# Kernel optimization log

Hardware: AMD Instinct MI355X
Metric: run time of the kernel (lower is better)

Reference implementation:

```python
import jax, jax.numpy as jnp
import numpy as np

HIDDEN = 1024
N_HEADS = 16
HEAD_DIM = HIDDEN // N_HEADS
B, S = 4, 4096


def setup_inputs() -> dict:
    key = jax.random.key(0)
    k1, k2, k3, k4, k5 = jax.random.split(key, 5)
    hidden_states = jax.random.normal(k1, (B, S, HIDDEN), dtype=jnp.float32)
    attention_mask = jnp.zeros((B, 1, 1, S), dtype=jnp.float32)
    scale = 1.0 / np.sqrt(HIDDEN)
    Wq = jax.random.normal(k2, (HIDDEN, HIDDEN), dtype=jnp.float32) * scale
    bq = jax.random.normal(k3, (HIDDEN,), dtype=jnp.float32) * 0.01
    Wkv = jax.random.normal(k4, (HIDDEN, HIDDEN), dtype=jnp.float32) * scale
    bkv = jax.random.normal(k5, (HIDDEN,), dtype=jnp.float32) * 0.01
    return {"hidden_states": hidden_states, "attention_mask": attention_mask,
            "Wq": Wq, "bq": bq, "Wkv": Wkv, "bkv": bkv}


def _split_heads(x, b, s):
    # [B, S, HIDDEN] -> [B, H, S, D]
    return x.reshape(b, s, N_HEADS, HEAD_DIM).transpose(0, 2, 1, 3)


def reference(hidden_states, attention_mask, Wq, bq, Wkv, bkv):
    b, s, _ = hidden_states.shape
    inv_sqrt_d = 1.0 / np.sqrt(HEAD_DIM)

    q = _split_heads(hidden_states @ Wq + bq, b, s)     # [B,H,S,D]
    k = _split_heads(hidden_states @ Wkv + bkv, b, s)   # [B,H,S,D]; value == key

    # ---- global token (index 0) attends to everything ----
    gq = q[:, :, 0:1, :]                                              # [B,H,1,D]
    g_scores = jnp.einsum('bhqd,bhkd->bhqk', gq, k) * inv_sqrt_d + attention_mask
    g_attn = jax.nn.softmax(g_scores, axis=-1)                        # [B,H,1,S]
    g_vec = jnp.einsum('bhqk,bhkd->bhqd', g_attn, k)                  # [B,H,1,D]

    # ---- local tokens 1..S-1: keys = [self, global_vec, prev, next(wrap to 0)] ----
    k_self = k[:, :, 1:, :]                                           # [B,H,S-1,D]
    k_glob = jnp.broadcast_to(g_vec, k_self.shape)                    # [B,H,S-1,D]
    k_prev = k[:, :, :-1, :]                                          # [B,H,S-1,D]
    k_next = jnp.concatenate([k[:, :, 2:, :], k[:, :, 0:1, :]], axis=2)
    keys4 = jnp.stack([k_self, k_glob, k_prev, k_next], axis=-1)      # [B,H,S-1,D,4]

    l_scores = jnp.einsum('bhsd,bhsdk->bhsk', q[:, :, 1:, :], keys4) * inv_sqrt_d
    l_attn = jax.nn.softmax(l_scores, axis=-1)                        # [B,H,S-1,4]
    l_vec = jnp.einsum('bhsk,bhsdk->bhsd', l_attn, keys4)             # [B,H,S-1,D]

    context = jnp.concatenate([g_vec, l_vec], axis=2)                 # [B,H,S,D]
    context = context.transpose(0, 2, 1, 3).reshape(b, s, N_HEADS * HEAD_DIM)
    return context, l_attn[:, :, :, None, :]                          # [B,H,S-1,1,4]
```

## Files before the change

### kernel.cpp

```cpp
#include <hip/hip_runtime.h>
#include <hip/hip_bf16.h>

#define NHEADS 16
#define HDIM   64
#define HID    1024
#define BB     4
#define SS     4096
#define MM     (BB*SS)
#define KK     HID
#define NN     (2*HID)

using short8 = __attribute__((ext_vector_type(8))) short;
using f32x4  = __attribute__((ext_vector_type(4))) float;

__device__ __forceinline__ float bf2f(ushort u) {
  return __uint_as_float(((unsigned)u) << 16);
}
__device__ __forceinline__ ushort f2bf(float f) {
  unsigned u = __float_as_uint(f);
  unsigned r = (u + 0x7fffu + ((u >> 16) & 1u)) >> 16;
  return (ushort)r;
}

__device__ __forceinline__ void gload16(const void* g, void* l) {
  __builtin_amdgcn_global_load_lds(
      (const __attribute__((address_space(1))) void*)g,
      (__attribute__((address_space(3))) void*)l, 16, 0, 0);
}

__global__ __launch_bounds__(256) void cast_hs_k(const float* __restrict__ in,
                                                 ushort* __restrict__ out) {
  size_t i = ((size_t)blockIdx.x * 256 + threadIdx.x) * 8;
  float4 a = *(const float4*)(in + i);
  float4 b = *(const float4*)(in + i + 4);
  ushort r[8];
  r[0]=f2bf(a.x); r[1]=f2bf(a.y); r[2]=f2bf(a.z); r[3]=f2bf(a.w);
  r[4]=f2bf(b.x); r[5]=f2bf(b.y); r[6]=f2bf(b.z); r[7]=f2bf(b.w);
  *(uint4*)(out + i) = *(const uint4*)r;
}

__global__ __launch_bounds__(256) void wcast_k(const float* __restrict__ Wq,
                                               const float* __restrict__ Wkv,
                                               ushort* __restrict__ Bt) {
  __shared__ float tile[32][33];
  int k0 = blockIdx.x * 32, n0 = blockIdx.y * 32;
  int tx = threadIdx.x, ty = threadIdx.y;
  const float* src = (n0 < HID) ? Wq : Wkv;
  int nc = (n0 < HID) ? n0 : n0 - HID;
#pragma unroll
  for (int j = 0; j < 4; ++j)
    tile[ty + 8*j][tx] = src[(size_t)(k0 + ty + 8*j) * HID + nc + tx];
  __syncthreads();
#pragma unroll
  for (int j = 0; j < 4; ++j)
    Bt[(size_t)(n0 + ty + 8*j) * KK + k0 + tx] = f2bf(tile[tx][ty + 8*j]);
}

__global__ __launch_bounds__(512, 2) void gemm_k(const ushort* __restrict__ A,
                                                 const ushort* __restrict__ Bt,
                                                 const float* __restrict__ bq,
                                                 const float* __restrict__ bkv,
                                                 ushort* __restrict__ C) {
  extern __shared__ char lds_c[];
  const int tid = threadIdx.x;
  const int bid = blockIdx.x;
  const int wg = (bid & 7) * 64 + (bid >> 3);
  const int tm = wg >> 3, tn = wg & 7;
  const int w = tid >> 6, lane = tid & 63;
  const int wr = w >> 2, wc = w & 3;
  const int lr = lane & 15, hi = lane >> 4;

  const ushort* Ab = A  + (size_t)tm * 256 * KK;
  const ushort* Bb = Bt + (size_t)tn * 256 * KK;

  const int d0 = tid * 16;
  const int gch = (tid & 3) ^ ((tid >> 3) & 3);
  const size_t soff0 = (size_t)(tid >> 2) * KK + gch * 8;
  const size_t soff1 = soff0 + (size_t)128 * KK;

  const int swz = (hi ^ ((lr >> 1) & 3)) << 4;
  const int arow = (wr * 128 + lr) * 64 + swz;
  const int brow = (wc * 64 + lr) * 64 + swz;

  f32x4 acc[8][4];
#pragma unroll
  for (int M = 0; M < 8; ++M)
#pragma unroll
    for (int n = 0; n < 4; ++n) acc[M][n] = (f32x4){0.f, 0.f, 0.f, 0.f};
  short8 bfrag[4];

#define STG(PANEL, KOFF, DSTB)                                                  \
  {                                                                             \
    const ushort* g_ = (PANEL) + (KOFF);                                        \
    gload16(g_ + soff0, lds_c + (DSTB) + d0);                                   \
    gload16(g_ + soff1, lds_c + (DSTB) + 8192 + d0);                            \
  }

#define LOADB(BBASE)                                                            \
  _Pragma("unroll") for (int n = 0; n < 4; ++n)                                 \
    bfrag[n] = *(const short8*)(lds_c + (BBASE) + n * 1024 + brow);

#define WAITV(N)                                                                \
  { asm volatile("s_waitcnt vmcnt(" #N ")" ::: "memory");                       \
    __builtin_amdgcn_sched_barrier(0); }

#define PH(ABASE, MH, STAGE_CODE, TAIL_CODE)                                    \
  {                                                                             \
    short8 afrag[4];                                                            \
    _Pragma("unroll") for (int m = 0; m < 4; ++m)                               \
      afrag[m] = *(const short8*)(lds_c + (ABASE) + (MH) * 4096 +               \
                                  m * 1024 + arow);                             \
    STAGE_CODE;                                                                 \
    __builtin_amdgcn_s_barrier();                                               \
    __builtin_amdgcn_sched_barrier(0);     \
    __builtin_amdgcn_s_setprio(1);                                              \
    _Pragma("unroll") for (int m = 0; m < 4; ++m)                               \
      _Pragma("unroll") for (int n = 0; n < 4; ++n)                             \
        acc[(MH) * 4 + m][n] = __builtin_amdgcn_mfma_f32_16x16x32_bf16(         \
            bfrag[n], afrag[m], acc[(MH) * 4 + m][n], 0, 0, 0);                 \
    __builtin_amdgcn_s_setprio(0);                                              \
    TAIL_CODE;                                                                  \
    __builtin_amdgcn_s_barrier();                                               \
    asm volatile("" ::: "memory");                                              \
  }

  STG(Bb, 0,   32768);
  STG(Ab, 0,   0);
  STG(Bb, 32,  49152);
  STG(Ab, 32,  16384);
  STG(Bb, 64,  98304);
  STG(Ab, 64,  65536);
  WAITV(8)
  __builtin_amdgcn_s_barrier();
  asm volatile("" ::: "memory");

#pragma unroll 1
  for (int it = 0; it < 7; ++it) {
    LOADB(32768)
    PH(0, 0, STG(Bb, (2 * it + 1) * 64 + 32, 114688), {})
    PH(0, 1, STG(Ab, (2 * it + 1) * 64 + 32, 81920), WAITV(8))
    LOADB(49152)
    PH(16384, 0, STG(Bb, (2 * it + 2) * 64, 32768), {})
    PH(16384, 1, STG(Ab, (2 * it + 2) * 64, 0), WAITV(8))
    LOADB(98304)
    PH(65536, 0, STG(Bb, (2 * it + 2) * 64 + 32, 49152), {})
    PH(65536, 1, STG(Ab, (2 * it + 2) * 64 + 32, 16384), WAITV(8))
    LOADB(114688)
    PH(81920, 0, STG(Bb, (2 * it + 3) * 64, 98304), {})
    PH(81920, 1, STG(Ab, (2 * it + 3) * 64, 65536), WAITV(8))
  }
  LOADB(32768)
  PH(0, 0, STG(Bb, 15 * 64 + 32, 114688), {})
  PH(0, 1, STG(Ab, 15 * 64 + 32, 81920), WAITV(8))
  LOADB(49152)
  PH(16384, 0, {}, {})
  PH(16384, 1, {}, WAITV(4))
  LOADB(98304)
  PH(65536, 0, {}, {})
  PH(65536, 1, {}, WAITV(0))
  LOADB(114688)
  PH(81920, 0, {}, {})
  PH(81920, 1, {}, {})

#undef PH
#undef WAITV
#undef LOADB
#undef STG

  const float* bias = (tn < 4) ? (bq + tn * 256) : (bkv + (tn - 4) * 256);
  float4 bv[4];
#pragma unroll
  for (int n = 0; n < 4; ++n)
    bv[n] = *(const float4*)(bias + wc * 64 + n * 16 + hi * 4);

#pragma unroll
  for (int M = 0; M < 8; ++M) {
    size_t row = (size_t)tm * 256 + wr * 128 + M * 16 + lr;
    ushort* cp = C + row * NN + tn * 256 + wc * 64 + hi * 4;
#pragma unroll
    for (int n = 0; n < 4; ++n) {
      unsigned p0 = (unsigned)f2bf(acc[M][n][0] + bv[n].x) |
                    ((unsigned)f2bf(acc[M][n][1] + bv[n].y) << 16);
      unsigned p1 = (unsigned)f2bf(acc[M][n][2] + bv[n].z) |
                    ((unsigned)f2bf(acc[M][n][3] + bv[n].w) << 16);
      uint2 st; st.x = p0; st.y = p1;
      *(uint2*)(cp + n * 16) = st;
    }
  }
}

#define GCH 8
#define GCS (SS / GCH)

__global__ __launch_bounds__(512) void gattn_part_k(const ushort* __restrict__ QK,
                                                    const float* __restrict__ mask,
                                                    float* __restrict__ P) {
  const int bh = blockIdx.x >> 3, c = blockIdx.x & 7;
  const int b = bh >> 4, h = bh & 15;
  const int tid = threadIdx.x, w = tid >> 6, lane = tid & 63;
  __shared__ float sc[GCS];
  __shared__ float red[8];
  __shared__ float vacc[8][64];

  const float gq = bf2f(QK[(size_t)b * SS * NN + h * HDIM + lane]);
  const int s0 = c * GCS;
  float mx = -1e30f;
  for (int s = w; s < GCS; s += 8) {
    float kv = bf2f(QK[((size_t)b * SS + s0 + s) * NN + HID + h * HDIM + lane]);
    float p = gq * kv;
#pragma unroll
    for (int o = 32; o; o >>= 1) p += __shfl_xor(p, o, 64);
    p = p * 0.125f + mask[b * SS + s0 + s];
    if (lane == 0) sc[s] = p;
    mx = fmaxf(mx, p);
  }
  if (lane == 0) red[w] = mx;
  __syncthreads();
  float bm = -1e30f;
#pragma unroll
  for (int i = 0; i < 8; ++i) bm = fmaxf(bm, red[i]);
  __syncthreads();
  float ls = 0.f;
  for (int s = tid; s < GCS; s += 512) {
    float e = __expf(sc[s] - bm);
    sc[s] = e;
    ls += e;
  }
#pragma unroll
  for (int o = 32; o; o >>= 1) ls += __shfl_xor(ls, o, 64);
  if (lane == 0) red[w] = ls;
  __syncthreads();
  float tot = 0.f;
#pragma unroll
  for (int i = 0; i < 8; ++i) tot += red[i];

  float a = 0.f;
  for (int s = w; s < GCS; s += 8)
    a += sc[s] * bf2f(QK[((size_t)b * SS + s0 + s) * NN + HID + h * HDIM + lane]);
  vacc[w][lane] = a;
  __syncthreads();
  if (w == 0) {
    float v = 0.f;
#pragma unroll
    for (int i = 0; i < 8; ++i) v += vacc[i][lane];
    P[1024 + (bh * 8 + c) * 64 + lane] = v;
    if (lane == 0) {
      P[bh * 8 + c] = bm;
      P[512 + bh * 8 + c] = tot;
    }
  }
}

__global__ __launch_bounds__(64) void gattn_comb_k(const float* __restrict__ P,
                                                   float* __restrict__ ctx,
                                                   float* __restrict__ gvec) {
  const int bh = blockIdx.x, b = bh >> 4, h = bh & 15;
  const int lane = threadIdx.x;
  float pm[8];
  float m = -1e30f;
#pragma unroll
  for (int c = 0; c < 8; ++c) { pm[c] = P[bh * 8 + c]; m = fmaxf(m, pm[c]); }
  float tot = 0.f, g = 0.f;
#pragma unroll
  for (int c = 0; c < 8; ++c) {
    float e = __expf(pm[c] - m);
    tot += P[512 + bh * 8 + c] * e;
    g += P[1024 + (bh * 8 + c) * 64 + lane] * e;
  }
  g /= tot;
  gvec[b * HID + h * HDIM + lane] = g;
  ctx[(size_t)b * SS * HID + h * HDIM + lane] = g;
}

__device__ __forceinline__ void unpack16(const ushort* __restrict__ p, float* f) {
  uint4 v0 = *(const uint4*)p;
  uint4 v1 = *(const uint4*)(p + 8);
  unsigned u[8] = {v0.x, v0.y, v0.z, v0.w, v1.x, v1.y, v1.z, v1.w};
#pragma unroll
  for (int i = 0; i < 8; ++i) {
    f[2*i]   = __uint_as_float(u[i] << 16);
    f[2*i+1] = __uint_as_float(u[i] & 0xffff0000u);
  }
}

__global__ __launch_bounds__(256) void local_attn_k(const ushort* __restrict__ QK,
                                                    const float* __restrict__ gvec,
                                                    float* __restrict__ out) {
  const int blk = blockIdx.x;
  const int b = blk >> 10;
  const int s = 1 + ((blk & 1023) << 2) + (int)(threadIdx.x >> 6);
  if (s >= SS) return;
  const int lane = threadIdx.x & 63;
  const int g = lane >> 2, j = lane & 3;
  const int db = g*HDIM + j*16;

  const size_t base = ((size_t)b*SS + s) * NN;
  const ushort* qp  = QK + base + db;
  const ushort* ksp = QK + base + HID + db;
  const ushort* kpp = QK + base - NN + HID + db;
  const int sn = (s == SS-1) ? 0 : s + 1;
  const ushort* knp = QK + ((size_t)b*SS + sn)*NN + HID + db;
  const float*  gvp = gvec + b*HID + db;

  float q[16], ks[16], kp[16], kn[16], gv[16];
  unpack16(qp, q); unpack16(ksp, ks); unpack16(kpp, kp); unpack16(knp, kn);
#pragma unroll
  for (int t = 0; t < 16; t += 4) *(float4*)(gv + t) = *(const float4*)(gvp + t);

  float d0=0.f, d1=0.f, d2=0.f, d3=0.f;
#pragma unroll
  for (int t = 0; t < 16; ++t) {
    d0 += q[t]*ks[t]; d1 += q[t]*gv[t]; d2 += q[t]*kp[t]; d3 += q[t]*kn[t];
  }
  d0 += __shfl_xor(d0, 1, 64); d0 += __shfl_xor(d0, 2, 64);
  d1 += __shfl_xor(d1, 1, 64); d1 += __shfl_xor(d1, 2, 64);
  d2 += __shfl_xor(d2, 1, 64); d2 += __shfl_xor(d2, 2, 64);
  d3 += __shfl_xor(d3, 1, 64); d3 += __shfl_xor(d3, 2, 64);

  float s0 = d0*0.125f, s1 = d1*0.125f, s2 = d2*0.125f, s3 = d3*0.125f;
  float m = fmaxf(fmaxf(s0, s1), fmaxf(s2, s3));
  float e0 = __expf(s0 - m), e1 = __expf(s1 - m), e2 = __expf(s2 - m), e3 = __expf(s3 - m);
  float inv = 1.f / (e0 + e1 + e2 + e3);
  float a0 = e0*inv, a1 = e1*inv, a2 = e2*inv, a3 = e3*inv;

  float o[16];
#pragma unroll
  for (int t = 0; t < 16; ++t) o[t] = a0*ks[t] + a1*gv[t] + a2*kp[t] + a3*kn[t];
  float* cp = out + ((size_t)b*SS + s)*HID + db;
#pragma unroll
  for (int t = 0; t < 16; t += 4) *(float4*)(cp + t) = *(const float4*)(o + t);

  if (j == 0) {
    float4 av; av.x = a0; av.y = a1; av.z = a2; av.w = a3;
    *(float4*)(out + (size_t)BB*SS*HID + (((size_t)b*NHEADS + g)*(SS-1) + (s-1))*4) = av;
  }
}

extern "C" void kernel_launch(void* const* d_in, const int* in_sizes, int n_in,
                              void* d_out, int out_size, void* d_ws, size_t ws_size,
                              hipStream_t stream) {
  const float* hs   = (const float*)d_in[0];
  const float* mask = (const float*)d_in[1];
  const float* Wq   = (const float*)d_in[2];
  const float* bq   = (const float*)d_in[3];
  const float* Wkv  = (const float*)d_in[4];
  const float* bkv  = (const float*)d_in[5];
  float* out = (float*)d_out;

  char* ws = (char*)d_ws;
  ushort* hsb  = (ushort*)ws;
  ushort* Bt   = (ushort*)(ws + 33554432);
  ushort* QK   = (ushort*)(ws + 33554432 + 4194304);
  float*  gvec = (float*)(ws + 33554432 + 4194304 + 67108864);
  float*  P    = (float*)(ws + 33554432 + 4194304 + 67108864 + 16384);

  cast_hs_k<<<MM*KK/(256*8), 256, 0, stream>>>(hs, hsb);
  wcast_k<<<dim3(KK/32, NN/32), dim3(32, 8), 0, stream>>>(Wq, Wkv, Bt);
  gemm_k<<<dim3((MM/256)*(NN/256)), dim3(512), 131072, stream>>>(hsb, Bt, bq, bkv, QK);
  gattn_part_k<<<BB*NHEADS*GCH, 512, 0, stream>>>(QK, mask, P);
  gattn_comb_k<<<BB*NHEADS, 64, 0, stream>>>(P, out, gvec);
  local_attn_k<<<BB*1024, 256, 0, stream>>>(QK, gvec, out);
}
```

Measured before the change: 176.1 us.

## Pre-pack operands into MFMA fragment layout and load GEMM fragments directly from global

The cast kernels now write hidden states and weights as bf16 in a fragment-major layout that matches the 16x16x32 MFMA operand order. The GEMM drops its LDS staging, barriers and hand-scheduled pipeline, and instead loads each wave's A/B fragments directly from global memory into double-buffered registers. This removes LDS traffic and synchronization. In exchange, each block gets no shared reuse across waves, so L2/global traffic is duplicated and there is less latency hiding.

```diff
diff --git a/kernel.cpp b/kernel.cpp
--- a/kernel.cpp
+++ b/kernel.cpp
@@ -22,150 +22,93 @@
   return (ushort)r;
 }
 
-__device__ __forceinline__ void gload16(const void* g, void* l) {
-  __builtin_amdgcn_global_load_lds(
-      (const __attribute__((address_space(1))) void*)g,
-      (__attribute__((address_space(3))) void*)l, 16, 0, 0);
-}
-
-__global__ __launch_bounds__(256) void cast_hs_k(const float* __restrict__ in,
-                                                 ushort* __restrict__ out) {
-  size_t i = ((size_t)blockIdx.x * 256 + threadIdx.x) * 8;
-  float4 a = *(const float4*)(in + i);
-  float4 b = *(const float4*)(in + i + 4);
+__global__ __launch_bounds__(256) void af_cast_k(const float* __restrict__ hs,
+                                                 ushort* __restrict__ Af) {
+  const int t = threadIdx.x;
+  const int U = blockIdx.x * 4 + (t >> 6);
+  const int l = t & 63, lr = l & 15, hi = l >> 4;
+  const int mt = U >> 5, g = U & 31;
+  const float* src = hs + (size_t)(mt * 16 + lr) * HID + g * 32 + hi * 8;
+  float4 x = *(const float4*)src;
+  float4 y = *(const float4*)(src + 4);
   ushort r[8];
-  r[0]=f2bf(a.x); r[1]=f2bf(a.y); r[2]=f2bf(a.z); r[3]=f2bf(a.w);
-  r[4]=f2bf(b.x); r[5]=f2bf(b.y); r[6]=f2bf(b.z); r[7]=f2bf(b.w);
-  *(uint4*)(out + i) = *(const uint4*)r;
-}
-
-__global__ __launch_bounds__(256) void wcast_k(const float* __restrict__ Wq,
-                                               const float* __restrict__ Wkv,
-                                               ushort* __restrict__ Bt) {
+  r[0]=f2bf(x.x); r[1]=f2bf(x.y); r[2]=f2bf(x.z); r[3]=f2bf(x.w);
+  r[4]=f2bf(y.x); r[5]=f2bf(y.y); r[6]=f2bf(y.z); r[7]=f2bf(y.w);
+  *(uint4*)(Af + (size_t)U * 512 + l * 8) = *(const uint4*)r;
+}
+
+__global__ __launch_bounds__(256) void wf_cast_k(const float* __restrict__ Wq,
+                                                 const float* __restrict__ Wkv,
+                                                 ushort* __restrict__ Bf) {
   __shared__ float tile[32][33];
-  int k0 = blockIdx.x * 32, n0 = blockIdx.y * 32;
-  int tx = threadIdx.x, ty = threadIdx.y;
+  const int k0 = blockIdx.x * 32, n0 = blockIdx.y * 32;
+  const int tx = threadIdx.x & 31, ty = threadIdx.x >> 5;
   const float* src = (n0 < HID) ? Wq : Wkv;
-  int nc = (n0 < HID) ? n0 : n0 - HID;
+  const int nc = (n0 < HID) ? n0 : n0 - HID;
 #pragma unroll
   for (int j = 0; j < 4; ++j)
     tile[ty + 8*j][tx] = src[(size_t)(k0 + ty + 8*j) * HID + nc + tx];
   __syncthreads();
-#pragma unroll
-  for (int j = 0; j < 4; ++j)
-    Bt[(size_t)(n0 + ty + 8*j) * KK + k0 + tx] = f2bf(tile[tx][ty + 8*j]);
-}
-
-__global__ __launch_bounds__(512, 2) void gemm_k(const ushort* __restrict__ A,
-                                                 const ushort* __restrict__ Bt,
+  const int t = threadIdx.x;
+  if (t < 128) {
+    const int l = t & 63, h = t >> 6, lr = l & 15, hi = l >> 4;
+    const int nt = (n0 >> 4) + h, g = k0 >> 5;
+    ushort r[8];
+#pragma unroll
+    for (int e = 0; e < 8; ++e) r[e] = f2bf(tile[hi*8 + e][h*16 + lr]);
+    *(uint4*)(Bf + (size_t)(nt * 32 + g) * 512 + l * 8) = *(const uint4*)r;
+  }
+}
+
+__global__ __launch_bounds__(512, 2) void gemm_k(const ushort* __restrict__ Af,
+                                                 const ushort* __restrict__ Bf,
                                                  const float* __restrict__ bq,
                                                  const float* __restrict__ bkv,
                                                  ushort* __restrict__ C) {
-  extern __shared__ char lds_c[];
-  const int tid = threadIdx.x;
-  const int bid = blockIdx.x;
+  const int tid = threadIdx.x, bid = blockIdx.x;
   const int wg = (bid & 7) * 64 + (bid >> 3);
   const int tm = wg >> 3, tn = wg & 7;
   const int w = tid >> 6, lane = tid & 63;
   const int wr = w >> 2, wc = w & 3;
   const int lr = lane & 15, hi = lane >> 4;
 
-  const ushort* Ab = A  + (size_t)tm * 256 * KK;
-  const ushort* Bb = Bt + (size_t)tn * 256 * KK;
-
-  const int d0 = tid * 16;
-  const int gch = (tid & 3) ^ ((tid >> 3) & 3);
-  const size_t soff0 = (size_t)(tid >> 2) * KK + gch * 8;
-  const size_t soff1 = soff0 + (size_t)128 * KK;
-
-  const int swz = (hi ^ ((lr >> 1) & 3)) << 4;
-  const int arow = (wr * 128 + lr) * 64 + swz;
-  const int brow = (wc * 64 + lr) * 64 + swz;
+  const ushort* aB = Af + (size_t)(tm * 16 + wr * 8) * 16384 + lane * 8;
+  const ushort* bB = Bf + (size_t)(tn * 16 + wc * 4) * 16384 + lane * 8;
 
   f32x4 acc[8][4];
 #pragma unroll
   for (int M = 0; M < 8; ++M)
 #pragma unroll
     for (int n = 0; n < 4; ++n) acc[M][n] = (f32x4){0.f, 0.f, 0.f, 0.f};
-  short8 bfrag[4];
-
-#define STG(PANEL, KOFF, DSTB)                                                  \
-  {                                                                             \
-    const ushort* g_ = (PANEL) + (KOFF);                                        \
-    gload16(g_ + soff0, lds_c + (DSTB) + d0);                                   \
-    gload16(g_ + soff1, lds_c + (DSTB) + 8192 + d0);                            \
-  }
-
-#define LOADB(BBASE)                                                            \
+
+  short8 a0[8], a1[8], b0[4], b1[4];
+
+#define LDA(SET, G)                                                             \
+  _Pragma("unroll") for (int m = 0; m < 8; ++m)                                 \
+    SET[m] = *(const short8*)(aB + m * 16384 + (G) * 512);
+#define LDB(SET, G)                                                             \
   _Pragma("unroll") for (int n = 0; n < 4; ++n)                                 \
-    bfrag[n] = *(const short8*)(lds_c + (BBASE) + n * 1024 + brow);
-
-#define WAITV(N)                                                                \
-  { asm volatile("s_waitcnt vmcnt(" #N ")" ::: "memory");                       \
-    __builtin_amdgcn_sched_barrier(0); }
-
-#define PH(ABASE, MH, STAGE_CODE, TAIL_CODE)                                    \
-  {                                                                             \
-    short8 afrag[4];                                                            \
-    _Pragma("unroll") for (int m = 0; m < 4; ++m)                               \
-      afrag[m] = *(const short8*)(lds_c + (ABASE) + (MH) * 4096 +               \
-                                  m * 1024 + arow);                             \
-    STAGE_CODE;                                                                 \
-    __builtin_amdgcn_s_barrier();                                               \
-    __builtin_amdgcn_sched_barrier(0);     \
-    __builtin_amdgcn_s_setprio(1);                                              \
-    _Pragma("unroll") for (int m = 0; m < 4; ++m)                               \
-      _Pragma("unroll") for (int n = 0; n < 4; ++n)                             \
-        acc[(MH) * 4 + m][n] = __builtin_amdgcn_mfma_f32_16x16x32_bf16(         \
-            bfrag[n], afrag[m], acc[(MH) * 4 + m][n], 0, 0, 0);                 \
-    __builtin_amdgcn_s_setprio(0);                                              \
-    TAIL_CODE;                                                                  \
-    __builtin_amdgcn_s_barrier();                                               \
-    asm volatile("" ::: "memory");                                              \
-  }
-
-  STG(Bb, 0,   32768);
-  STG(Ab, 0,   0);
-  STG(Bb, 32,  49152);
-  STG(Ab, 32,  16384);
-  STG(Bb, 64,  98304);
-  STG(Ab, 64,  65536);
-  WAITV(8)
-  __builtin_amdgcn_s_barrier();
-  asm volatile("" ::: "memory");
+    SET[n] = *(const short8*)(bB + n * 16384 + (G) * 512);
+#define MFM(AS, BS)                                                             \
+  _Pragma("unroll") for (int m = 0; m < 8; ++m)                                 \
+    _Pragma("unroll") for (int n = 0; n < 4; ++n)                               \
+      acc[m][n] = __builtin_amdgcn_mfma_f32_16x16x32_bf16(BS[n], AS[m],         \
+                                                          acc[m][n], 0, 0, 0);
+
+  LDA(a0, 0) LDB(b0, 0)
+  LDA(a1, 1) LDB(b1, 1)
 
 #pragma unroll 1
-  for (int it = 0; it < 7; ++it) {
-    LOADB(32768)
-    PH(0, 0, STG(Bb, (2 * it + 1) * 64 + 32, 114688), {})
-    PH(0, 1, STG(Ab, (2 * it + 1) * 64 + 32, 81920), WAITV(8))
-    LOADB(49152)
-    PH(16384, 0, STG(Bb, (2 * it + 2) * 64, 32768), {})
-    PH(16384, 1, STG(Ab, (2 * it + 2) * 64, 0), WAITV(8))
-    LOADB(98304)
-    PH(65536, 0, STG(Bb, (2 * it + 2) * 64 + 32, 49152), {})
-    PH(65536, 1, STG(Ab, (2 * it + 2) * 64 + 32, 16384), WAITV(8))
-    LOADB(114688)
-    PH(81920, 0, STG(Bb, (2 * it + 3) * 64, 98304), {})
-    PH(81920, 1, STG(Ab, (2 * it + 3) * 64, 65536), WAITV(8))
-  }
-  LOADB(32768)
-  PH(0, 0, STG(Bb, 15 * 64 + 32, 114688), {})
-  PH(0, 1, STG(Ab, 15 * 64 + 32, 81920), WAITV(8))
-  LOADB(49152)
-  PH(16384, 0, {}, {})
-  PH(16384, 1, {}, WAITV(4))
-  LOADB(98304)
-  PH(65536, 0, {}, {})
-  PH(65536, 1, {}, WAITV(0))
-  LOADB(114688)
-  PH(81920, 0, {}, {})
-  PH(81920, 1, {}, {})
-
-#undef PH
-#undef WAITV
-#undef LOADB
-#undef STG
+  for (int g = 0; g < 32; g += 2) {
+    MFM(a0, b0)
+    LDA(a0, g + 2) LDB(b0, g + 2)
+    MFM(a1, b1)
+    LDA(a1, g + 3) LDB(b1, g + 3)
+  }
+
+#undef MFM
+#undef LDB
+#undef LDA
 
   const float* bias = (tn < 4) ? (bq + tn * 256) : (bkv + (tn - 4) * 256);
   float4 bv[4];
@@ -348,15 +291,15 @@
   float* out = (float*)d_out;
 
   char* ws = (char*)d_ws;
-  ushort* hsb  = (ushort*)ws;
-  ushort* Bt   = (ushort*)(ws + 33554432);
+  ushort* Af   = (ushort*)ws;
+  ushort* Bf   = (ushort*)(ws + 33554432);
   ushort* QK   = (ushort*)(ws + 33554432 + 4194304);
   float*  gvec = (float*)(ws + 33554432 + 4194304 + 67108864);
   float*  P    = (float*)(ws + 33554432 + 4194304 + 67108864 + 16384);
 
-  cast_hs_k<<<MM*KK/(256*8), 256, 0, stream>>>(hs, hsb);
-  wcast_k<<<dim3(KK/32, NN/32), dim3(32, 8), 0, stream>>>(Wq, Wkv, Bt);
-  gemm_k<<<dim3((MM/256)*(NN/256)), dim3(512), 131072, stream>>>(hsb, Bt, bq, bkv, QK);
+  af_cast_k<<<8192, 256, 0, stream>>>(hs, Af);
+  wf_cast_k<<<dim3(KK/32, NN/32), 256, 0, stream>>>(Wq, Wkv, Bf);
+  gemm_k<<<512, 512, 0, stream>>>(Af, Bf, bq, bkv, QK);
   gattn_part_k<<<BB*NHEADS*GCH, 512, 0, stream>>>(QK, mask, P);
   gattn_comb_k<<<BB*NHEADS, 64, 0, stream>>>(P, out, gvec);
   local_attn_k<<<BB*1024, 256, 0, stream>>>(QK, gvec, out);
```

New measurement: 178.2 us. Within noise of the previous version (+1.2%).
